# Performance work log

Measured on AMD Instinct MI355X. Metric: run time of the kernel, lower is better.

## Reference

```python
import jax, jax.numpy as jnp
import numpy as np

BIT = 4
HALF = 2 ** (BIT - 1)          # 8 -> signed integer grid [-8, 7]
N_LEVELS = 2 ** BIT - 1        # 15
COUT, CIN, KH, KW = 1024, 1024, 3, 3


def _flip_pass(r, err, up_num, up_err, up_pri, dn_num, dn_err, dn_pri):
    """One SQuant flip pass over rows (groups). Greedily flips the rounding
    direction of the highest-priority elements so each row's rounding-error
    sum becomes ~0, and hands off boundary priorities for the next pass
    (reconstruction of the SQuant_func CUDA kernel)."""
    G, K = r.shape
    rows = jnp.arange(G)
    e = err.sum(-1)                                    # (G,) error budget
    nflip = jnp.round(jnp.abs(e)).astype(jnp.int32)    # flips needed per row
    is_up = e < 0                                      # under-rounded -> flip up

    pri = jnp.where(is_up[:, None], up_pri, dn_pri)
    order = jnp.argsort(-pri, axis=-1)                 # descending priority
    rank = jnp.zeros((G, K), jnp.int32).at[rows[:, None], order].set(
        jnp.broadcast_to(jnp.arange(K, dtype=jnp.int32), (G, K)))
    flip = rank < nflip[:, None]

    cand_num = jnp.where(is_up[:, None], up_num, dn_num)
    cand_err = jnp.where(is_up[:, None], up_err, dn_err)
    new_r = jnp.where(flip, cand_num, r)
    new_err = jnp.where(flip, cand_err, err)

    # ---- boundary-priority handoff for the next (channel-wise) pass ----
    ni = jnp.take_along_axis(order, jnp.clip(nflip, 0, K - 1)[:, None], axis=-1)[:, 0]      # next candidate
    li = jnp.take_along_axis(order, jnp.clip(nflip - 1, 0, K - 1)[:, None], axis=-1)[:, 0]  # last flipped
    has_next = nflip < K
    has_last = nflip > 0
    next_pri = jnp.where(has_next, pri[rows, ni], 0.0)         # flip one more element
    last_pri = jnp.where(has_last, 1.0 - pri[rows, li], 0.0)   # revert the last flip

    z = jnp.zeros_like(pri)
    new_up_pri = z.at[rows, ni].add(jnp.where(is_up, next_pri, 0.0))
    new_up_pri = new_up_pri.at[rows, li].add(jnp.where(~is_up, last_pri, 0.0))
    new_dn_pri = z.at[rows, ni].add(jnp.where(~is_up, next_pri, 0.0))
    new_dn_pri = new_dn_pri.at[rows, li].add(jnp.where(is_up, last_pri, 0.0))

    # reverting the last flipped element restores its pre-flip value/error
    up_last = is_up & has_last
    dn_last = (~is_up) & has_last
    new_dn_num = dn_num.at[rows, li].set(jnp.where(up_last, r[rows, li], dn_num[rows, li]))
    new_dn_err = dn_err.at[rows, li].set(jnp.where(up_last, err[rows, li], dn_err[rows, li]))
    new_up_num = up_num.at[rows, li].set(jnp.where(dn_last, r[rows, li], up_num[rows, li]))
    new_up_err = up_err.at[rows, li].set(jnp.where(dn_last, err[rows, li], up_err[rows, li]))
    return new_r, new_err, new_up_num, new_up_err, new_up_pri, new_dn_num, new_dn_err, new_dn_pri


def _adaptive_round(q):
    t_min, t_max = float(-HALF), float(HALF - 1)
    r = jnp.round(q)
    err = r - q
    cand_up = (err < 0) & (q < t_max)    # elements that may be rounded up instead
    cand_dn = (err > 0) & (q > t_min)    # elements that may be rounded down instead
    up_num = jnp.where(cand_up, r + 1.0, r)
    up_err = jnp.where(cand_up, err + 1.0, 0.0)
    up_pri = jnp.where(cand_up, -err, 0.0)   # |rounding error|
    dn_num = jnp.where(cand_dn, r - 1.0, r)
    dn_err = jnp.where(cand_dn, err - 1.0, 0.0)
    dn_pri = jnp.where(cand_dn, err, 0.0)

    cout, cin = q.shape[0], q.shape[1]
    k = q.size // (cout * cin)
    st = tuple(a.reshape(cout * cin, k) for a in (r, err, up_num, up_err, up_pri, dn_num, dn_err, dn_pri))
    st = _flip_pass(*st)                               # SQuant-K: per (Cout,Cin) kernel
    st = tuple(a.reshape(cout, cin * k) for a in st)
    st = _flip_pass(*st)                               # SQuant-C: per output channel
    return st[0].reshape(q.shape)


def _squant_quantize(weight):
    flat = weight.reshape(weight.shape[0], -1)
    x_max = flat.max(1)
    x_min = flat.min(1)
    scale = N_LEVELS / jnp.maximum(x_max - x_min, 1e-8)   # asymmetric per-channel
    zp = jnp.round(scale * x_min) + HALF                  # signed, integral zero point
    bshape = (-1,) + (1,) * (weight.ndim - 1)
    scale = scale.reshape(bshape)
    zp = zp.reshape(bshape)
    q = scale * weight - zp                               # linear_quantize
    q = _adaptive_round(q)
    q = jnp.clip(q, -HALF, HALF - 1)
    return (q + zp) / scale                               # linear_dequantize


def setup_inputs() -> dict:
    key = jax.random.key(0)
    weight = jax.random.normal(key, (COUT, CIN, KH, KW), dtype=jnp.float32) * 0.05
    return {"weight": weight}


def reference(weight):
    return _squant_quantize(weight)
```

## Files before the change

### kernel.cpp

```cpp
#include <hip/hip_runtime.h>

#define NROW   1024
#define ROWLEN 9216
#define NGRP   1024
#define NT     512
#define GPT    2
#define NLEAF  128
#define LCAP   256

__device__ __forceinline__ int bucketOf(float v) {
    int b = (int)(v * 256.0f);
    return b > 255 ? 255 : b;
}

__global__ __launch_bounds__(NT, 4) void squant_kernel(const float* __restrict__ w,
                                                       float* __restrict__ out) {
    __shared__ float4 s_buf4[ROWLEN / 4];
    __shared__ signed char s_r2[ROWLEN];
    __shared__ unsigned short s_upos[NGRP];
    __shared__ unsigned short s_dpos[NGRP];
    __shared__ float s_uval[NGRP];
    __shared__ float s_dval[NGRP];
    __shared__ signed char s_ucn[NGRP];
    __shared__ signed char s_dcn[NGRP];
    __shared__ float s_leaf[NLEAF];
    __shared__ int   s_hist[256];
    __shared__ float s_lv[LCAP];
    __shared__ unsigned short s_lg[LCAP];
    __shared__ float s_wred[16];
    __shared__ float s_bc[2];
    __shared__ int   s_seli[2];
    __shared__ int   s_lcount;

    float* s_err = (float*)s_buf4;
    const int row = blockIdx.x;
    const int tid = threadIdx.x;
    const int lane = tid & 63, wid = tid >> 6;
    const float* wrow = w + (size_t)row * ROWLEN;

    float vmin =  3.402823466e38f;
    float vmax = -3.402823466e38f;
    const float4* w4 = reinterpret_cast<const float4*>(wrow);
    #pragma unroll
    for (int k = 0; k < 4; ++k) {
        int i = tid + k * NT;
        float4 v = w4[i];
        s_buf4[i] = v;
        vmin = fminf(vmin, fminf(fminf(v.x, v.y), fminf(v.z, v.w)));
        vmax = fmaxf(vmax, fmaxf(fmaxf(v.x, v.y), fmaxf(v.z, v.w)));
    }
    if (tid < 256) {
        int i = 2048 + tid;
        float4 v = w4[i];
        s_buf4[i] = v;
        vmin = fminf(vmin, fminf(fminf(v.x, v.y), fminf(v.z, v.w)));
        vmax = fmaxf(vmax, fmaxf(fmaxf(v.x, v.y), fmaxf(v.z, v.w)));
    }
    #pragma unroll
    for (int o = 32; o > 0; o >>= 1) {
        vmin = fminf(vmin, __shfl_xor(vmin, o, 64));
        vmax = fmaxf(vmax, __shfl_xor(vmax, o, 64));
    }
    if (lane == 0) { s_wred[wid] = vmin; s_wred[8 + wid] = vmax; }
    __syncthreads();
    if (tid == 0) {
        float a = s_wred[0], b = s_wred[8];
        #pragma unroll
        for (int i = 1; i < 8; ++i) { a = fminf(a, s_wred[i]); b = fmaxf(b, s_wred[8 + i]); }
        s_bc[0] = a; s_bc[1] = b;
    }
    __syncthreads();

    const float xmin  = s_bc[0];
    const float xmax  = s_bc[1];
    const float scale = __fdiv_rn(15.0f, fmaxf(__fsub_rn(xmax, xmin), 1e-8f));
    const float zp    = __fadd_rn(rintf(__fmul_rn(scale, xmin)), 8.0f);

    for (int gi = 0; gi < GPT; ++gi) {
        const int g = tid * GPT + gi;
        const int base = g * 9;
        float q[9], r[9], err[9], pri[9];
        #pragma unroll
        for (int j = 0; j < 9; ++j) {
            float wv = s_err[base + j];
            float qq = __fsub_rn(__fmul_rn(scale, wv), zp);
            float rr = rintf(qq);
            q[j] = qq; r[j] = rr; err[j] = __fsub_rn(rr, qq);
        }
        float e = __fadd_rn(
                    __fadd_rn(__fadd_rn(__fadd_rn(err[0], err[1]), __fadd_rn(err[2], err[3])),
                              __fadd_rn(__fadd_rn(err[4], err[5]), __fadd_rn(err[6], err[7]))),
                    err[8]);
        int nflip = (int)rintf(fabsf(e));
        const bool isup = (e < 0.0f);
        #pragma unroll
        for (int j = 0; j < 9; ++j) {
            bool cand = isup ? ((err[j] < 0.0f) && (q[j] < 7.0f))
                             : ((err[j] > 0.0f) && (q[j] > -8.0f));
            pri[j] = cand ? (isup ? -err[j] : err[j]) : 0.0f;
        }
        int rank[9] = {0,0,0,0,0,0,0,0,0};
        #pragma unroll
        for (int a = 0; a < 9; ++a)
            #pragma unroll
            for (int b = a + 1; b < 9; ++b) {
                int c = (pri[a] >= pri[b]) ? 1 : 0;
                rank[b] += c;
                rank[a] += 1 - c;
            }
        const int nf  = nflip < 9 ? nflip : 9;
        const int nip = nf < 8 ? nf : 8;
        int lip = nf - 1; if (lip < 0) lip = 0;

        int ni = 0, li = 0;
        float pri_ni = 0.0f, pri_li = 0.0f, r_ni = 0.0f, r_li = 0.0f;
        #pragma unroll
        for (int j = 0; j < 9; ++j) {
            bool cand = pri[j] > 0.0f;
            bool flip = rank[j] < nf;
            float cnj = cand ? (isup ? r[j] + 1.0f : r[j] - 1.0f) : r[j];
            float cej = cand ? (isup ? __fadd_rn(err[j], 1.0f) : __fsub_rn(err[j], 1.0f)) : 0.0f;
            s_r2[base + j]  = (signed char)__float2int_rn(flip ? cnj : r[j]);
            s_err[base + j] = flip ? cej : err[j];
            if (rank[j] == nip) { ni = j; pri_ni = pri[j]; r_ni = r[j]; }
            if (rank[j] == lip) { li = j; pri_li = pri[j]; r_li = r[j]; }
        }
        const bool has_next = (nflip < 9);
        const bool has_last = (nflip > 0);
        const float next_pri = has_next ? pri_ni : 0.0f;
        const float last_pri = has_last ? __fsub_rn(1.0f, pri_li) : 0.0f;
        signed char ncv = (signed char)__float2int_rn(
            (pri_ni > 0.0f) ? (isup ? r_ni + 1.0f : r_ni - 1.0f) : r_ni);
        signed char lcv = (signed char)__float2int_rn(r_li);
        if (isup) {
            s_upos[g] = (unsigned short)(base + ni); s_uval[g] = next_pri; s_ucn[g] = ncv;
            s_dpos[g] = (unsigned short)(base + li); s_dval[g] = last_pri; s_dcn[g] = lcv;
        } else {
            s_dpos[g] = (unsigned short)(base + ni); s_dval[g] = next_pri; s_dcn[g] = ncv;
            s_upos[g] = (unsigned short)(base + li); s_uval[g] = last_pri; s_ucn[g] = lcv;
        }
    }
    __syncthreads();

    if (tid < NLEAF) {
        const float* a = s_err + tid * 72;
        float acc[8];
        #pragma unroll
        for (int j = 0; j < 8; ++j) acc[j] = a[j];
        for (int i = 8; i < 72; i += 8) {
            #pragma unroll
            for (int j = 0; j < 8; ++j) acc[j] = __fadd_rn(acc[j], a[i + j]);
        }
        s_leaf[tid] = __fadd_rn(__fadd_rn(__fadd_rn(acc[0], acc[1]), __fadd_rn(acc[2], acc[3])),
                                __fadd_rn(__fadd_rn(acc[4], acc[5]), __fadd_rn(acc[6], acc[7])));
    }
    __syncthreads();
    for (int s = 1; s < NLEAF; s <<= 1) {
        if (tid < NLEAF && (tid & (2 * s - 1)) == 0)
            s_leaf[tid] = __fadd_rn(s_leaf[tid], s_leaf[tid + s]);
        __syncthreads();
    }
    const float e2     = s_leaf[0];
    const int   nflip2 = (int)rintf(fabsf(e2));
    const bool  isup2  = (e2 < 0.0f);

    const float* val = isup2 ? s_uval : s_dval;
    const unsigned short* pos = isup2 ? s_upos : s_dpos;
    const signed char* cnv = isup2 ? s_ucn : s_dcn;

    if (tid < 256) s_hist[tid] = 0;
    if (tid == 0) s_lcount = 0;
    __syncthreads();

    const int g0 = tid, g1 = tid + NT;
    const float v0 = val[g0], v1 = val[g1];
    const int b0 = (v0 > 0.0f) ? bucketOf(v0) : -1;
    const int b1 = (v1 > 0.0f) ? bucketOf(v1) : -1;
    if (b0 >= 0) atomicAdd(&s_hist[b0], 1);
    if (b1 >= 0) atomicAdd(&s_hist[b1], 1);
    __syncthreads();
    for (int s = 1; s < 256; s <<= 1) {
        int t = 0;
        if (tid < 256) t = s_hist[tid] + ((tid + s < 256) ? s_hist[tid + s] : 0);
        __syncthreads();
        if (tid < 256) s_hist[tid] = t;
        __syncthreads();
    }
    const int npos = s_hist[0];

    if (nflip2 > 0 && nflip2 <= npos) {
        if (tid < 256) {
            int Tb  = s_hist[tid];
            int Tb1 = (tid < 255) ? s_hist[tid + 1] : 0;
            if (Tb >= nflip2 && Tb1 < nflip2) { s_seli[0] = tid; s_seli[1] = nflip2 - Tb1; }
        }
        __syncthreads();
        const int B = s_seli[0], m = s_seli[1];
        if (b0 > B) s_r2[pos[g0]] = cnv[g0];
        else if (b0 == B) { int ix = atomicAdd(&s_lcount, 1);
                            if (ix < LCAP) { s_lv[ix] = v0; s_lg[ix] = (unsigned short)g0; } }
        if (b1 > B) s_r2[pos[g1]] = cnv[g1];
        else if (b1 == B) { int ix = atomicAdd(&s_lcount, 1);
                            if (ix < LCAP) { s_lv[ix] = v1; s_lg[ix] = (unsigned short)g1; } }
        __syncthreads();
        const int L = s_lcount;
        if (L <= LCAP) {
            if (b0 == B) {
                int rk = 0;
                for (int l = 0; l < L; ++l) {
                    float lv = s_lv[l]; int lg = s_lg[l];
                    rk += (int)((lv > v0) || ((lv == v0) && (lg < g0)));
                }
                if (rk < m) s_r2[pos[g0]] = cnv[g0];
            }
            if (b1 == B) {
                int rk = 0;
                for (int l = 0; l < L; ++l) {
                    float lv = s_lv[l]; int lg = s_lg[l];
                    rk += (int)((lv > v1) || ((lv == v1) && (lg < g1)));
                }
                if (rk < m) s_r2[pos[g1]] = cnv[g1];
            }
        } else {
            if (b0 == B) {
                int rk = 0;
                for (int j = 0; j < NGRP; ++j) {
                    float vj = val[j];
                    if (vj > 0.0f && bucketOf(vj) == B)
                        rk += (int)((vj > v0) || ((vj == v0) && (j < g0)));
                }
                if (rk < m) s_r2[pos[g0]] = cnv[g0];
            }
            if (b1 == B) {
                int rk = 0;
                for (int j = 0; j < NGRP; ++j) {
                    float vj = val[j];
                    if (vj > 0.0f && bucketOf(vj) == B)
                        rk += (int)((vj > v1) || ((vj == v1) && (j < g1)));
                }
                if (rk < m) s_r2[pos[g1]] = cnv[g1];
            }
        }
    } else if (nflip2 > npos) {
        if (b0 >= 0) s_r2[pos[g0]] = cnv[g0];
        if (b1 >= 0) s_r2[pos[g1]] = cnv[g1];
        const int extra = nflip2 - npos;
        signed char*  s_upn  = (signed char*)s_err;
        signed char*  s_dnn  = (signed char*)s_err + ROWLEN;
        unsigned char* s_flag = (unsigned char*)s_err + 2 * ROWLEN;
        for (int i = tid; i < ROWLEN; i += NT) s_flag[i] = 0;
        __syncthreads();
        for (int gi = 0; gi < GPT; ++gi) {
            const int base = (tid * GPT + gi) * 9;
            float q[9], r[9], err[9], pri[9];
            #pragma unroll
            for (int j = 0; j < 9; ++j) {
                float wv = wrow[base + j];
                float qq = __fsub_rn(__fmul_rn(scale, wv), zp);
                float rr = rintf(qq);
                q[j] = qq; r[j] = rr; err[j] = __fsub_rn(rr, qq);
            }
            float e = __fadd_rn(
                        __fadd_rn(__fadd_rn(__fadd_rn(err[0], err[1]), __fadd_rn(err[2], err[3])),
                                  __fadd_rn(__fadd_rn(err[4], err[5]), __fadd_rn(err[6], err[7]))),
                        err[8]);
            int nflip = (int)rintf(fabsf(e));
            const bool isup = (e < 0.0f);
            #pragma unroll
            for (int j = 0; j < 9; ++j) {
                bool cand = isup ? ((err[j] < 0.0f) && (q[j] < 7.0f))
                                 : ((err[j] > 0.0f) && (q[j] > -8.0f));
                pri[j] = cand ? (isup ? -err[j] : err[j]) : 0.0f;
            }
            int rank[9] = {0,0,0,0,0,0,0,0,0};
            #pragma unroll
            for (int a = 0; a < 9; ++a)
                #pragma unroll
                for (int b = a + 1; b < 9; ++b) {
                    int c = (pri[a] >= pri[b]) ? 1 : 0;
                    rank[b] += c; rank[a] += 1 - c;
                }
            const int nf = nflip < 9 ? nflip : 9;
            int lip = nf - 1; if (lip < 0) lip = 0;
            int li = 0;
            #pragma unroll
            for (int j = 0; j < 9; ++j) {
                bool cu = (err[j] < 0.0f) && (q[j] < 7.0f);
                bool cd = (err[j] > 0.0f) && (q[j] > -8.0f);
                s_upn[base + j] = (signed char)__float2int_rn(cu ? r[j] + 1.0f : r[j]);
                s_dnn[base + j] = (signed char)__float2int_rn(cd ? r[j] - 1.0f : r[j]);
                if (rank[j] == lip) li = j;
            }
            if (nflip > 0) {
                if (isup) s_dnn[base + li] = (signed char)__float2int_rn(r[li]);
                else      s_upn[base + li] = (signed char)__float2int_rn(r[li]);
            }
        }
        for (int e2i = tid; e2i < NGRP; e2i += NT)
            if (val[e2i] > 0.0f) s_flag[pos[e2i]] = 1;
        __syncthreads();
        if (tid == 0) {
            int c = 0;
            for (int p = 0; p < ROWLEN && c < extra; ++p)
                if (!s_flag[p]) { s_r2[p] = isup2 ? s_upn[p] : s_dnn[p]; ++c; }
        }
    }
    __syncthreads();

    float4* o4 = reinterpret_cast<float4*>(out + (size_t)row * ROWLEN);
    #pragma unroll
    for (int k = 0; k < 5; ++k) {
        int i = tid + k * NT;
        if (k == 4 && tid >= 256) break;
        int b = i * 4;
        int v0i = s_r2[b + 0], v1i = s_r2[b + 1], v2i = s_r2[b + 2], v3i = s_r2[b + 3];
        v0i = v0i < -8 ? -8 : (v0i > 7 ? 7 : v0i);
        v1i = v1i < -8 ? -8 : (v1i > 7 ? 7 : v1i);
        v2i = v2i < -8 ? -8 : (v2i > 7 ? 7 : v2i);
        v3i = v3i < -8 ? -8 : (v3i > 7 ? 7 : v3i);
        float4 o;
        o.x = __fdiv_rn(__fadd_rn((float)v0i, zp), scale);
        o.y = __fdiv_rn(__fadd_rn((float)v1i, zp), scale);
        o.z = __fdiv_rn(__fadd_rn((float)v2i, zp), scale);
        o.w = __fdiv_rn(__fadd_rn((float)v3i, zp), scale);
        o4[i] = o;
    }
}

extern "C" void kernel_launch(void* const* d_in, const int* in_sizes, int n_in,
                              void* d_out, int out_size, void* d_ws, size_t ws_size,
                              hipStream_t stream) {
    const float* w = (const float*)d_in[0];
    float* out = (float*)d_out;
    squant_kernel<<<dim3(NROW), dim3(NT), 0, stream>>>(w, out);
}
```

Baseline: 105.6 us.

## Drop shared float error buffer, recompute errors from global loads, halve block size

Removes the 36KB shared float buffer holding weights and errors. Per-element errors are now recomputed from a second global/L2 read of the row plus an encoded int8 state (offset by 100 for a flip of a non-candidate). The block shrinks to 256 threads with 4 groups each, and the tree reductions and prefix scan become wavefront shuffles. The aim is to cut LDS use to raise occupancy and to remove barriers. The cost is re-reading global memory and a serial replay inside the rare fallback path.

```diff
diff --git a/kernel.cpp b/kernel.cpp
--- a/kernel.cpp
+++ b/kernel.cpp
@@ -3,9 +3,8 @@
 #define NROW   1024
 #define ROWLEN 9216
 #define NGRP   1024
-#define NT     512
-#define GPT    2
-#define NLEAF  128
+#define NT     256
+#define GPT    4
 #define LCAP   256
 
 __device__ __forceinline__ int bucketOf(float v) {
@@ -13,26 +12,72 @@
     return b > 255 ? 255 : b;
 }
 
-__global__ __launch_bounds__(NT, 4) void squant_kernel(const float* __restrict__ w,
+__device__ __forceinline__ float err2_of(float wv, int enc, float scale, float zp) {
+    float q = __fsub_rn(__fmul_rn(scale, wv), zp);
+    float r = rintf(q);
+    float err = __fsub_rn(r, q);
+    if (enc > 50) return 0.0f;
+    int delta = enc - __float2int_rn(r);
+    return delta ? __fadd_rn(err, (float)delta) : err;
+}
+
+__device__ void replay_group(const float* wg, float scale, float zp,
+                             float r[9], float err[9], float q[9],
+                             int* nflip1, bool* isup1, int* li_out) {
+    float pri[9];
+    #pragma unroll
+    for (int j = 0; j < 9; ++j) {
+        float qq = __fsub_rn(__fmul_rn(scale, wg[j]), zp);
+        float rr = rintf(qq);
+        q[j] = qq; r[j] = rr; err[j] = __fsub_rn(rr, qq);
+    }
+    float e = __fadd_rn(
+                __fadd_rn(__fadd_rn(__fadd_rn(err[0], err[1]), __fadd_rn(err[2], err[3])),
+                          __fadd_rn(__fadd_rn(err[4], err[5]), __fadd_rn(err[6], err[7]))),
+                err[8]);
+    int nf0 = (int)rintf(fabsf(e));
+    bool up = (e < 0.0f);
+    #pragma unroll
+    for (int j = 0; j < 9; ++j) {
+        bool cand = up ? ((err[j] < 0.0f) && (q[j] < 7.0f))
+                       : ((err[j] > 0.0f) && (q[j] > -8.0f));
+        pri[j] = cand ? (up ? -err[j] : err[j]) : 0.0f;
+    }
+    int rank[9] = {0,0,0,0,0,0,0,0,0};
+    #pragma unroll
+    for (int a = 0; a < 9; ++a)
+        #pragma unroll
+        for (int b = a + 1; b < 9; ++b) {
+            int c = (pri[a] >= pri[b]) ? 1 : 0;
+            rank[b] += c; rank[a] += 1 - c;
+        }
+    int nf = nf0 < 9 ? nf0 : 9;
+    int lip = nf - 1; if (lip < 0) lip = 0;
+    int li = 0;
+    #pragma unroll
+    for (int j = 0; j < 9; ++j) if (rank[j] == lip) li = j;
+    *nflip1 = nf0; *isup1 = up; *li_out = li;
+}
+
+__global__ __launch_bounds__(NT, 5) void squant_kernel(const float* __restrict__ w,
                                                        float* __restrict__ out) {
-    __shared__ float4 s_buf4[ROWLEN / 4];
-    __shared__ signed char s_r2[ROWLEN];
+    __shared__ alignas(16) signed char s_r2[ROWLEN];
     __shared__ unsigned short s_upos[NGRP];
     __shared__ unsigned short s_dpos[NGRP];
     __shared__ float s_uval[NGRP];
     __shared__ float s_dval[NGRP];
     __shared__ signed char s_ucn[NGRP];
     __shared__ signed char s_dcn[NGRP];
-    __shared__ float s_leaf[NLEAF];
+    __shared__ float s_leaf[128];
     __shared__ int   s_hist[256];
     __shared__ float s_lv[LCAP];
     __shared__ unsigned short s_lg[LCAP];
-    __shared__ float s_wred[16];
+    __shared__ float s_wred[8];
     __shared__ float s_bc[2];
+    __shared__ float s_e2s;
     __shared__ int   s_seli[2];
     __shared__ int   s_lcount;
 
-    float* s_err = (float*)s_buf4;
     const int row = blockIdx.x;
     const int tid = threadIdx.x;
     const int lane = tid & 63, wid = tid >> 6;
@@ -42,17 +87,8 @@
     float vmax = -3.402823466e38f;
     const float4* w4 = reinterpret_cast<const float4*>(wrow);
     #pragma unroll
-    for (int k = 0; k < 4; ++k) {
-        int i = tid + k * NT;
-        float4 v = w4[i];
-        s_buf4[i] = v;
-        vmin = fminf(vmin, fminf(fminf(v.x, v.y), fminf(v.z, v.w)));
-        vmax = fmaxf(vmax, fmaxf(fmaxf(v.x, v.y), fmaxf(v.z, v.w)));
-    }
-    if (tid < 256) {
-        int i = 2048 + tid;
-        float4 v = w4[i];
-        s_buf4[i] = v;
+    for (int k = 0; k < 9; ++k) {
+        float4 v = w4[tid + k * NT];
         vmin = fminf(vmin, fminf(fminf(v.x, v.y), fminf(v.z, v.w)));
         vmax = fmaxf(vmax, fmaxf(fmaxf(v.x, v.y), fmaxf(v.z, v.w)));
     }
@@ -61,28 +97,30 @@
         vmin = fminf(vmin, __shfl_xor(vmin, o, 64));
         vmax = fmaxf(vmax, __shfl_xor(vmax, o, 64));
     }
-    if (lane == 0) { s_wred[wid] = vmin; s_wred[8 + wid] = vmax; }
+    if (lane == 0) { s_wred[wid] = vmin; s_wred[4 + wid] = vmax; }
     __syncthreads();
     if (tid == 0) {
-        float a = s_wred[0], b = s_wred[8];
-        #pragma unroll
-        for (int i = 1; i < 8; ++i) { a = fminf(a, s_wred[i]); b = fmaxf(b, s_wred[8 + i]); }
+        float a = s_wred[0], b = s_wred[4];
+        #pragma unroll
+        for (int i = 1; i < 4; ++i) { a = fminf(a, s_wred[i]); b = fmaxf(b, s_wred[4 + i]); }
         s_bc[0] = a; s_bc[1] = b;
     }
     __syncthreads();
-
-    const float xmin  = s_bc[0];
-    const float xmax  = s_bc[1];
-    const float scale = __fdiv_rn(15.0f, fmaxf(__fsub_rn(xmax, xmin), 1e-8f));
-    const float zp    = __fadd_rn(rintf(__fmul_rn(scale, xmin)), 8.0f);
-
+    const float scale = __fdiv_rn(15.0f, fmaxf(__fsub_rn(s_bc[1], s_bc[0]), 1e-8f));
+    const float zp    = __fadd_rn(rintf(__fmul_rn(scale, s_bc[0])), 8.0f);
+
+    const float4* wt4 = reinterpret_cast<const float4*>(wrow + 36 * tid);
+    #pragma unroll
     for (int gi = 0; gi < GPT; ++gi) {
         const int g = tid * GPT + gi;
         const int base = g * 9;
+        const int a4 = (9 * gi) >> 2;
+        float4 A = wt4[a4], B = wt4[a4 + 1], C = wt4[a4 + 2];
+        float f[12] = {A.x, A.y, A.z, A.w, B.x, B.y, B.z, B.w, C.x, C.y, C.z, C.w};
         float q[9], r[9], err[9], pri[9];
         #pragma unroll
         for (int j = 0; j < 9; ++j) {
-            float wv = s_err[base + j];
+            float wv = f[gi + j];
             float qq = __fsub_rn(__fmul_rn(scale, wv), zp);
             float rr = rintf(qq);
             q[j] = qq; r[j] = rr; err[j] = __fsub_rn(rr, qq);
@@ -105,8 +143,7 @@
             #pragma unroll
             for (int b = a + 1; b < 9; ++b) {
                 int c = (pri[a] >= pri[b]) ? 1 : 0;
-                rank[b] += c;
-                rank[a] += 1 - c;
+                rank[b] += c; rank[a] += 1 - c;
             }
         const int nf  = nflip < 9 ? nflip : 9;
         const int nip = nf < 8 ? nf : 8;
@@ -119,9 +156,9 @@
             bool cand = pri[j] > 0.0f;
             bool flip = rank[j] < nf;
             float cnj = cand ? (isup ? r[j] + 1.0f : r[j] - 1.0f) : r[j];
-            float cej = cand ? (isup ? __fadd_rn(err[j], 1.0f) : __fsub_rn(err[j], 1.0f)) : 0.0f;
-            s_r2[base + j]  = (signed char)__float2int_rn(flip ? cnj : r[j]);
-            s_err[base + j] = flip ? cej : err[j];
+            int enc = __float2int_rn(flip ? cnj : r[j]);
+            if (flip && !cand) enc += 100;
+            s_r2[base + j] = (signed char)enc;
             if (rank[j] == nip) { ni = j; pri_ni = pri[j]; r_ni = r[j]; }
             if (rank[j] == lip) { li = j; pri_li = pri[j]; r_li = r[j]; }
         }
@@ -142,187 +179,160 @@
     }
     __syncthreads();
 
-    if (tid < NLEAF) {
-        const float* a = s_err + tid * 72;
-        float acc[8];
-        #pragma unroll
-        for (int j = 0; j < 8; ++j) acc[j] = a[j];
-        for (int i = 8; i < 72; i += 8) {
-            #pragma unroll
-            for (int j = 0; j < 8; ++j) acc[j] = __fadd_rn(acc[j], a[i + j]);
-        }
-        s_leaf[tid] = __fadd_rn(__fadd_rn(__fadd_rn(acc[0], acc[1]), __fadd_rn(acc[2], acc[3])),
-                                __fadd_rn(__fadd_rn(acc[4], acc[5]), __fadd_rn(acc[6], acc[7])));
-    }
-    __syncthreads();
-    for (int s = 1; s < NLEAF; s <<= 1) {
-        if (tid < NLEAF && (tid & (2 * s - 1)) == 0)
-            s_leaf[tid] = __fadd_rn(s_leaf[tid], s_leaf[tid + s]);
-        __syncthreads();
-    }
-    const float e2     = s_leaf[0];
+    {
+        const int l = tid >> 1, h = tid & 1;
+        float a0, a1, a2, a3;
+        #pragma unroll
+        for (int i = 0; i < 9; ++i) {
+            const int off = 72 * l + 8 * i + 4 * h;
+            float4 v = *reinterpret_cast<const float4*>(wrow + off);
+            int e4 = *reinterpret_cast<const int*>(s_r2 + off);
+            float e0 = err2_of(v.x, (int)(signed char)(e4 & 0xff),         scale, zp);
+            float e1 = err2_of(v.y, (int)(signed char)((e4 >> 8) & 0xff),  scale, zp);
+            float e2v= err2_of(v.z, (int)(signed char)((e4 >> 16) & 0xff), scale, zp);
+            float e3 = err2_of(v.w, (int)(signed char)((e4 >> 24) & 0xff), scale, zp);
+            if (i == 0) { a0 = e0; a1 = e1; a2 = e2v; a3 = e3; }
+            else {
+                a0 = __fadd_rn(a0, e0); a1 = __fadd_rn(a1, e1);
+                a2 = __fadd_rn(a2, e2v); a3 = __fadd_rn(a3, e3);
+            }
+        }
+        float t = __fadd_rn(__fadd_rn(a0, a1), __fadd_rn(a2, a3));
+        float o = __shfl_xor(t, 1, 64);
+        if (h == 0) s_leaf[l] = __fadd_rn(t, o);
+        s_hist[tid] = 0;
+        if (tid == 0) s_lcount = 0;
+    }
+    __syncthreads();
+    if (tid < 64) {
+        float v = __fadd_rn(s_leaf[2 * tid], s_leaf[2 * tid + 1]);
+        #pragma unroll
+        for (int o = 1; o < 64; o <<= 1) {
+            float u = __shfl_xor(v, o, 64);
+            v = __fadd_rn(v, u);
+        }
+        if (tid == 0) s_e2s = v;
+    }
+    __syncthreads();
+
+    const float e2     = s_e2s;
     const int   nflip2 = (int)rintf(fabsf(e2));
     const bool  isup2  = (e2 < 0.0f);
-
     const float* val = isup2 ? s_uval : s_dval;
     const unsigned short* pos = isup2 ? s_upos : s_dpos;
     const signed char* cnv = isup2 ? s_ucn : s_dcn;
 
-    if (tid < 256) s_hist[tid] = 0;
-    if (tid == 0) s_lcount = 0;
-    __syncthreads();
-
-    const int g0 = tid, g1 = tid + NT;
-    const float v0 = val[g0], v1 = val[g1];
-    const int b0 = (v0 > 0.0f) ? bucketOf(v0) : -1;
-    const int b1 = (v1 > 0.0f) ? bucketOf(v1) : -1;
-    if (b0 >= 0) atomicAdd(&s_hist[b0], 1);
-    if (b1 >= 0) atomicAdd(&s_hist[b1], 1);
-    __syncthreads();
-    for (int s = 1; s < 256; s <<= 1) {
-        int t = 0;
-        if (tid < 256) t = s_hist[tid] + ((tid + s < 256) ? s_hist[tid + s] : 0);
-        __syncthreads();
-        if (tid < 256) s_hist[tid] = t;
-        __syncthreads();
-    }
+    int   gg[4]; float vv[4]; int bb[4];
+    #pragma unroll
+    for (int m = 0; m < 4; ++m) {
+        gg[m] = tid + m * NT;
+        vv[m] = val[gg[m]];
+        bb[m] = (vv[m] > 0.0f) ? bucketOf(vv[m]) : -1;
+        if (bb[m] >= 0) atomicAdd(&s_hist[bb[m]], 1);
+    }
+    __syncthreads();
+    if (tid < 64) {
+        int b0 = s_hist[4*tid], b1 = s_hist[4*tid+1], b2 = s_hist[4*tid+2], b3 = s_hist[4*tid+3];
+        int s3 = b3, s2 = b2 + s3, s1 = b1 + s2, s0 = b0 + s1;
+        int suf = s0;
+        #pragma unroll
+        for (int off = 1; off < 64; off <<= 1) {
+            int o = __shfl_down(suf, off, 64);
+            if (tid + off < 64) suf += o;
+        }
+        int above = suf - s0;
+        s_hist[4*tid]   = s0 + above;
+        s_hist[4*tid+1] = s1 + above;
+        s_hist[4*tid+2] = s2 + above;
+        s_hist[4*tid+3] = s3 + above;
+    }
+    __syncthreads();
     const int npos = s_hist[0];
 
     if (nflip2 > 0 && nflip2 <= npos) {
-        if (tid < 256) {
+        {
             int Tb  = s_hist[tid];
             int Tb1 = (tid < 255) ? s_hist[tid + 1] : 0;
             if (Tb >= nflip2 && Tb1 < nflip2) { s_seli[0] = tid; s_seli[1] = nflip2 - Tb1; }
         }
         __syncthreads();
         const int B = s_seli[0], m = s_seli[1];
-        if (b0 > B) s_r2[pos[g0]] = cnv[g0];
-        else if (b0 == B) { int ix = atomicAdd(&s_lcount, 1);
-                            if (ix < LCAP) { s_lv[ix] = v0; s_lg[ix] = (unsigned short)g0; } }
-        if (b1 > B) s_r2[pos[g1]] = cnv[g1];
-        else if (b1 == B) { int ix = atomicAdd(&s_lcount, 1);
-                            if (ix < LCAP) { s_lv[ix] = v1; s_lg[ix] = (unsigned short)g1; } }
+        #pragma unroll
+        for (int mm = 0; mm < 4; ++mm) {
+            if (bb[mm] > B) s_r2[pos[gg[mm]]] = cnv[gg[mm]];
+            else if (bb[mm] == B) {
+                int ix = atomicAdd(&s_lcount, 1);
+                if (ix < LCAP) { s_lv[ix] = vv[mm]; s_lg[ix] = (unsigned short)gg[mm]; }
+            }
+        }
         __syncthreads();
         const int L = s_lcount;
         if (L <= LCAP) {
-            if (b0 == B) {
+            #pragma unroll
+            for (int mm = 0; mm < 4; ++mm) {
+                if (bb[mm] != B) continue;
                 int rk = 0;
                 for (int l = 0; l < L; ++l) {
                     float lv = s_lv[l]; int lg = s_lg[l];
-                    rk += (int)((lv > v0) || ((lv == v0) && (lg < g0)));
+                    rk += (int)((lv > vv[mm]) || ((lv == vv[mm]) && (lg < gg[mm])));
                 }
-                if (rk < m) s_r2[pos[g0]] = cnv[g0];
-            }
-            if (b1 == B) {
-                int rk = 0;
-                for (int l = 0; l < L; ++l) {
-                    float lv = s_lv[l]; int lg = s_lg[l];
-                    rk += (int)((lv > v1) || ((lv == v1) && (lg < g1)));
-                }
-                if (rk < m) s_r2[pos[g1]] = cnv[g1];
+                if (rk < m) s_r2[pos[gg[mm]]] = cnv[gg[mm]];
             }
         } else {
-            if (b0 == B) {
+            #pragma unroll
+            for (int mm = 0; mm < 4; ++mm) {
+                if (bb[mm] != B) continue;
                 int rk = 0;
                 for (int j = 0; j < NGRP; ++j) {
                     float vj = val[j];
                     if (vj > 0.0f && bucketOf(vj) == B)
-                        rk += (int)((vj > v0) || ((vj == v0) && (j < g0)));
+                        rk += (int)((vj > vv[mm]) || ((vj == vv[mm]) && (j < gg[mm])));
                 }
-                if (rk < m) s_r2[pos[g0]] = cnv[g0];
-            }
-            if (b1 == B) {
-                int rk = 0;
-                for (int j = 0; j < NGRP; ++j) {
-                    float vj = val[j];
-                    if (vj > 0.0f && bucketOf(vj) == B)
-                        rk += (int)((vj > v1) || ((vj == v1) && (j < g1)));
-                }
-                if (rk < m) s_r2[pos[g1]] = cnv[g1];
+                if (rk < m) s_r2[pos[gg[mm]]] = cnv[gg[mm]];
             }
         }
     } else if (nflip2 > npos) {
-        if (b0 >= 0) s_r2[pos[g0]] = cnv[g0];
-        if (b1 >= 0) s_r2[pos[g1]] = cnv[g1];
-        const int extra = nflip2 - npos;
-        signed char*  s_upn  = (signed char*)s_err;
-        signed char*  s_dnn  = (signed char*)s_err + ROWLEN;
-        unsigned char* s_flag = (unsigned char*)s_err + 2 * ROWLEN;
-        for (int i = tid; i < ROWLEN; i += NT) s_flag[i] = 0;
-        __syncthreads();
-        for (int gi = 0; gi < GPT; ++gi) {
-            const int base = (tid * GPT + gi) * 9;
-            float q[9], r[9], err[9], pri[9];
-            #pragma unroll
-            for (int j = 0; j < 9; ++j) {
-                float wv = wrow[base + j];
-                float qq = __fsub_rn(__fmul_rn(scale, wv), zp);
-                float rr = rintf(qq);
-                q[j] = qq; r[j] = rr; err[j] = __fsub_rn(rr, qq);
-            }
-            float e = __fadd_rn(
-                        __fadd_rn(__fadd_rn(__fadd_rn(err[0], err[1]), __fadd_rn(err[2], err[3])),
-                                  __fadd_rn(__fadd_rn(err[4], err[5]), __fadd_rn(err[6], err[7]))),
-                        err[8]);
-            int nflip = (int)rintf(fabsf(e));
-            const bool isup = (e < 0.0f);
-            #pragma unroll
-            for (int j = 0; j < 9; ++j) {
-                bool cand = isup ? ((err[j] < 0.0f) && (q[j] < 7.0f))
-                                 : ((err[j] > 0.0f) && (q[j] > -8.0f));
-                pri[j] = cand ? (isup ? -err[j] : err[j]) : 0.0f;
-            }
-            int rank[9] = {0,0,0,0,0,0,0,0,0};
-            #pragma unroll
-            for (int a = 0; a < 9; ++a)
-                #pragma unroll
-                for (int b = a + 1; b < 9; ++b) {
-                    int c = (pri[a] >= pri[b]) ? 1 : 0;
-                    rank[b] += c; rank[a] += 1 - c;
-                }
-            const int nf = nflip < 9 ? nflip : 9;
-            int lip = nf - 1; if (lip < 0) lip = 0;
-            int li = 0;
-            #pragma unroll
-            for (int j = 0; j < 9; ++j) {
-                bool cu = (err[j] < 0.0f) && (q[j] < 7.0f);
-                bool cd = (err[j] > 0.0f) && (q[j] > -8.0f);
-                s_upn[base + j] = (signed char)__float2int_rn(cu ? r[j] + 1.0f : r[j]);
-                s_dnn[base + j] = (signed char)__float2int_rn(cd ? r[j] - 1.0f : r[j]);
-                if (rank[j] == lip) li = j;
-            }
-            if (nflip > 0) {
-                if (isup) s_dnn[base + li] = (signed char)__float2int_rn(r[li]);
-                else      s_upn[base + li] = (signed char)__float2int_rn(r[li]);
-            }
-        }
-        for (int e2i = tid; e2i < NGRP; e2i += NT)
-            if (val[e2i] > 0.0f) s_flag[pos[e2i]] = 1;
+        #pragma unroll
+        for (int mm = 0; mm < 4; ++mm)
+            if (bb[mm] >= 0) s_r2[pos[gg[mm]]] = cnv[gg[mm]];
         __syncthreads();
         if (tid == 0) {
-            int c = 0;
-            for (int p = 0; p < ROWLEN && c < extra; ++p)
-                if (!s_flag[p]) { s_r2[p] = isup2 ? s_upn[p] : s_dnn[p]; ++c; }
-        }
-    }
-    __syncthreads();
-
+            int c = 0; const int extra = nflip2 - npos;
+            for (int g = 0; g < NGRP && c < extra; ++g) {
+                float r[9], err[9], q[9]; int nf1; bool up1; int li;
+                replay_group(wrow + 9 * g, scale, zp, r, err, q, &nf1, &up1, &li);
+                for (int j = 0; j < 9 && c < extra; ++j) {
+                    int p = 9 * g + j;
+                    if (val[g] > 0.0f && pos[g] == p) continue;
+                    float cnp;
+                    if (isup2) { bool cu = (err[j] < 0.0f) && (q[j] < 7.0f);
+                                 cnp = cu ? r[j] + 1.0f : r[j]; }
+                    else       { bool cd = (err[j] > 0.0f) && (q[j] > -8.0f);
+                                 cnp = cd ? r[j] - 1.0f : r[j]; }
+                    if (nf1 > 0 && j == li && (up1 != isup2)) cnp = r[j];
+                    s_r2[p] = (signed char)__float2int_rn(cnp);
+                    ++c;
+                }
+            }
+        }
+    }
+    __syncthreads();
+
+    const int* r2i = reinterpret_cast<const int*>(s_r2);
     float4* o4 = reinterpret_cast<float4*>(out + (size_t)row * ROWLEN);
     #pragma unroll
-    for (int k = 0; k < 5; ++k) {
+    for (int k = 0; k < 9; ++k) {
         int i = tid + k * NT;
-        if (k == 4 && tid >= 256) break;
-        int b = i * 4;
-        int v0i = s_r2[b + 0], v1i = s_r2[b + 1], v2i = s_r2[b + 2], v3i = s_r2[b + 3];
-        v0i = v0i < -8 ? -8 : (v0i > 7 ? 7 : v0i);
-        v1i = v1i < -8 ? -8 : (v1i > 7 ? 7 : v1i);
-        v2i = v2i < -8 ? -8 : (v2i > 7 ? 7 : v2i);
-        v3i = v3i < -8 ? -8 : (v3i > 7 ? 7 : v3i);
+        int word = r2i[i];
         float4 o;
-        o.x = __fdiv_rn(__fadd_rn((float)v0i, zp), scale);
-        o.y = __fdiv_rn(__fadd_rn((float)v1i, zp), scale);
-        o.z = __fdiv_rn(__fadd_rn((float)v2i, zp), scale);
-        o.w = __fdiv_rn(__fadd_rn((float)v3i, zp), scale);
+        #pragma unroll
+        for (int c = 0; c < 4; ++c) {
+            int v = (int)(signed char)((word >> (8 * c)) & 0xff);
+            if (v > 50) v -= 100;
+            v = v < -8 ? -8 : (v > 7 ? 7 : v);
+            float f = __fdiv_rn(__fadd_rn((float)v, zp), scale);
+            if (c == 0) o.x = f; else if (c == 1) o.y = f; else if (c == 2) o.z = f; else o.w = f;
+        }
         o4[i] = o;
     }
 }
```

Result: slower. 109.3 us (+3.5%).
